# Optimization experiments

Hardware: AMD Instinct MI355X
Metric: run time of the kernel (lower is better)

Reference implementation:

```python
import jax, jax.numpy as jnp
import numpy as np

B, S, E, H = 2, 2048, 1024, 16
Dh = E // H  # 64
KEEP = 0.9   # 1 - dropout_p
INV_SCALE = 1.0  # forward() default; call site does not pass inv_scale


def setup_inputs() -> dict:
    key = jax.random.key(0)
    ks = jax.random.split(key, 12)
    query = jax.random.normal(ks[0], (B, S, E), dtype=jnp.float32)
    key_t = jax.random.normal(ks[1], (B, S, E), dtype=jnp.float32)
    value = jax.random.normal(ks[2], (B, S, E), dtype=jnp.float32)
    attn_mask = jax.random.randint(ks[3], (B, S), 0, 2, dtype=jnp.int32)
    # pre-scaled inverted dropout keep-mask (deterministic stand-in for F.dropout)
    dropout_mask = (jax.random.uniform(ks[4], (B, H, S, S)) < KEEP).astype(jnp.float32) / KEEP
    Wq = jax.random.normal(ks[5], (E, E), dtype=jnp.float32) * 0.02
    bq = jnp.zeros((E,), dtype=jnp.float32)
    Wk = jax.random.normal(ks[6], (E, E), dtype=jnp.float32) * 0.02
    bk = jnp.zeros((E,), dtype=jnp.float32)
    Wv = jax.random.normal(ks[7], (E, E), dtype=jnp.float32) * 0.02
    bv = jnp.zeros((E,), dtype=jnp.float32)
    return {"query": query, "key": key_t, "value": value, "attn_mask": attn_mask,
            "dropout_mask": dropout_mask, "Wq": Wq, "bq": bq, "Wk": Wk, "bk": bk,
            "Wv": Wv, "bv": bv}


def _heads(x, W, b):
    # Linear then split heads: (B,S,E) -> (B,H,S,Dh)
    y = x @ W.T + b
    return y.reshape(B, S, H, Dh).transpose(0, 2, 1, 3)


def reference(query, key, value, attn_mask, dropout_mask, Wq, bq, Wk, bk, Wv, bv):
    q = _heads(query, Wq, bq)
    k = _heads(key, Wk, bk)
    v = _heads(value, Wv, bv)
    scores = jnp.einsum("bhqd,bhkd->bhqk", q, k) / INV_SCALE
    pad = (attn_mask == 0)[:, None, None, :]  # (B,1,1,S) True = masked
    scores = jnp.where(pad, -jnp.inf, scores)
    attn = jax.nn.softmax(scores, axis=-1) * dropout_mask
    out = jnp.einsum("bhqk,bhkd->bhqd", attn, v)  # (B,H,S,Dh)
    return out
```

## Files before the change

### kernel.cpp

```cpp
#include <hip/hip_runtime.h>

#define B_ 2
#define S_ 2048
#define E_ 1024
#define H_ 16
#define DH 64
#define MM (B_*S_)
#define BHN (B_*H_)

typedef unsigned short u16;
typedef unsigned int u32;
typedef __attribute__((ext_vector_type(8))) __bf16 bf16x8;
typedef __attribute__((ext_vector_type(4))) float f32x4;
typedef __attribute__((ext_vector_type(8))) u16 u16x8;
typedef __attribute__((ext_vector_type(4))) u16 u16x4;

static __device__ __forceinline__ u16 f2bf(float f) {
  u32 u = __builtin_bit_cast(u32, f);
  u += 0x7fffu + ((u >> 16) & 1u);
  return (u16)(u >> 16);
}
static __device__ __forceinline__ float bf2f(u16 h) {
  return __builtin_bit_cast(float, (u32)h << 16);
}
static __device__ __forceinline__ u32 sw(u32 byte) {
  return byte ^ (((byte >> 7) & 7u) << 4);
}
static __device__ __forceinline__ void cp16(u16* lds, u32 ldsbyte, const u16* g) {
  *(u16x8*)((char*)lds + ldsbyte) = *(const u16x8*)g;
}
static __device__ __forceinline__ bf16x8 frag(const u16* lds, u32 byte) {
  return *(const bf16x8*)((const char*)lds + byte);
}
static __device__ __forceinline__ f32x4 mfma16(bf16x8 a, bf16x8 b, f32x4 c) {
  return __builtin_amdgcn_mfma_f32_16x16x32_bf16(a, b, c, 0, 0, 0);
}

__global__ void split3_kernel(const float* __restrict__ s0, u16* __restrict__ h0, u16* __restrict__ l0,
                              const float* __restrict__ s1, u16* __restrict__ h1, u16* __restrict__ l1,
                              const float* __restrict__ s2, u16* __restrict__ h2, u16* __restrict__ l2,
                              int n4) {
  const float* src = (blockIdx.z == 0) ? s0 : (blockIdx.z == 1) ? s1 : s2;
  u16* hi = (blockIdx.z == 0) ? h0 : (blockIdx.z == 1) ? h1 : h2;
  u16* lo = (blockIdx.z == 0) ? l0 : (blockIdx.z == 1) ? l1 : l2;
  int i = blockIdx.x * blockDim.x + threadIdx.x;
  int stride = gridDim.x * blockDim.x;
  for (; i < n4; i += stride) {
    float4 v = ((const float4*)src)[i];
    u16x4 h, l;
    h.x = f2bf(v.x); l.x = f2bf(v.x - bf2f(h.x));
    h.y = f2bf(v.y); l.y = f2bf(v.y - bf2f(h.y));
    h.z = f2bf(v.z); l.z = f2bf(v.z - bf2f(h.z));
    h.w = f2bf(v.w); l.w = f2bf(v.w - bf2f(h.w));
    ((u16x4*)hi)[i] = h;
    ((u16x4*)lo)[i] = l;
  }
}

struct ProjArgs {
  const u16* xhi; const u16* xlo; const u16* whi; const u16* wlo;
  const float* bias; u16* ohi; u16* olo; int mode;
};

__global__ __launch_bounds__(256, 2) void proj_gemm(ProjArgs a0, ProjArgs a1, ProjArgs a2) {
  ProjArgs A = (blockIdx.z == 0) ? a0 : (blockIdx.z == 1) ? a1 : a2;
  __shared__ u16 As[128 * 64];
  __shared__ u16 Bs[128 * 64];
  const int t = threadIdx.x;
  const int l = t & 63, wid = t >> 6;
  const int g = l >> 4, ln = l & 15;
  const int wm = wid >> 1, wn = wid & 1;
  const int m0 = blockIdx.y * 128, e0 = blockIdx.x * 128;

  f32x4 acc[4][4] = {};

  for (int kt = 0; kt < 48; ++kt) {
    int kp = kt * 64;
    const u16* asrc = (kp < 2048) ? A.xhi : A.xlo;
    const u16* bsrc = (kp < 1024 || kp >= 2048) ? A.whi : A.wlo;
    int kc = kp & 1023;
#pragma unroll
    for (int i = 0; i < 4; ++i) {
      int c = t + 256 * i;
      int row = c >> 3;
      u32 lb = sw((u32)c * 16);
      cp16(As, lb, asrc + (size_t)(m0 + row) * 1024 + kc + (c & 7) * 8);
      cp16(Bs, lb, bsrc + (size_t)(e0 + row) * 1024 + kc + (c & 7) * 8);
    }
    __syncthreads();
#pragma unroll
    for (int ks = 0; ks < 2; ++ks) {
      bf16x8 af[4], bfv[4];
#pragma unroll
      for (int i = 0; i < 4; ++i) {
        u32 ar = (u32)(wm * 64 + i * 16 + ln);
        af[i] = frag(As, sw(ar * 128 + g * 16 + ks * 64));
        u32 br = (u32)(wn * 64 + i * 16 + ln);
        bfv[i] = frag(Bs, sw(br * 128 + g * 16 + ks * 64));
      }
#pragma unroll
      for (int i = 0; i < 4; ++i)
#pragma unroll
        for (int j = 0; j < 4; ++j)
          acc[i][j] = mfma16(af[i], bfv[j], acc[i][j]);
    }
    __syncthreads();
  }

#pragma unroll
  for (int i = 0; i < 4; ++i) {
#pragma unroll
    for (int j = 0; j < 4; ++j) {
      int e = e0 + wn * 64 + j * 16 + ln;
      int h = e >> 6, d = e & 63;
      float bias = A.bias[e];
      if (A.mode < 2) {
#pragma unroll
        for (int r = 0; r < 4; ++r) {
          int m = m0 + wm * 64 + i * 16 + g * 4 + r;
          float v = acc[i][j][r] + bias;
          int b = m >> 11, s = m & 2047;
          size_t idx = ((size_t)((b * 16 + h) * 2048 + s)) * 64 + d;
          u16 hv = f2bf(v);
          A.ohi[idx] = hv;
          A.olo[idx] = f2bf(v - bf2f(hv));
        }
      } else {
        int m = m0 + wm * 64 + i * 16 + g * 4;
        int b = m >> 11, s = m & 2047;
        u16x4 pv;
#pragma unroll
        for (int r = 0; r < 4; ++r) pv[r] = f2bf(acc[i][j][r] + bias);
        size_t idx = ((size_t)((b * 16 + h) * 64 + d)) * 2048 + s;
        *(u16x4*)(A.ohi + idx) = pv;
      }
    }
  }
}

__global__ __launch_bounds__(256, 4) void attn_kernel(
    const u16* __restrict__ qhi, const u16* __restrict__ qlo,
    const u16* __restrict__ khi, const u16* __restrict__ klo,
    const u16* __restrict__ vt, const int* __restrict__ amask,
    const float* __restrict__ dmask, float* __restrict__ out) {
  __shared__ u16 Ksh[64 * 64];
  __shared__ u16 Ksl[64 * 64];
  __shared__ u16 Vs[64 * 64];
  __shared__ u16 Ps[4 * 16 * 64];

  const int t = threadIdx.x, l = t & 63, wid = t >> 6;
  const int g = l >> 4, ln = l & 15;

  int bid = blockIdx.y * 32 + blockIdx.x;
  int sid = (bid & 7) * 128 + (bid >> 3);
  const int qt = sid & 31, bh = sid >> 5, b = bh >> 4;
  const int q0 = qt * 64;
  const int qrow = q0 + wid * 16 + ln;
  const size_t qg = ((size_t)bh * 2048 + qrow) * 64;

  bf16x8 qh[2], ql[2];
#pragma unroll
  for (int ks = 0; ks < 2; ++ks) {
    qh[ks] = *(const bf16x8*)(qhi + qg + ks * 32 + g * 8);
    ql[ks] = *(const bf16x8*)(qlo + qg + ks * 32 + g * 8);
  }

  f32x4 O[4] = {};
  float Zacc = 0.f;
  const size_t dmrow = ((size_t)bh * 2048 + qrow) * 2048;
  const u32 psbase = (u32)(wid * 2048 + ln * 128);

  for (int kt = 0; kt < 32; ++kt) {
    const int k0 = kt * 64;
    float4 dm[4]; int4 ok[4];
#pragma unroll
    for (int i = 0; i < 4; ++i) {
      dm[i] = *(const float4*)(dmask + dmrow + k0 + i * 16 + 4 * g);
      ok[i] = *(const int4*)(amask + b * 2048 + k0 + i * 16 + 4 * g);
    }

    if (kt) __syncthreads();
    const size_t kbase = ((size_t)bh * 2048 + k0) * 64;
#pragma unroll
    for (int i = 0; i < 2; ++i) {
      int c = t + 256 * i;
      u32 lb = sw((u32)c * 16);
      int row = c >> 3;
      cp16(Ksh, lb, khi + kbase + c * 8);
      cp16(Ksl, lb, klo + kbase + c * 8);
      cp16(Vs, lb, vt + ((size_t)bh * 64 + row) * 2048 + k0 + (c & 7) * 8);
    }
    __syncthreads();

    f32x4 sc[4] = {};
#pragma unroll
    for (int ks = 0; ks < 2; ++ks) {
#pragma unroll
      for (int i = 0; i < 4; ++i) {
        u32 byt = sw((u32)((i * 16 + ln) * 128 + ks * 64 + g * 16));
        bf16x8 akh = frag(Ksh, byt);
        bf16x8 akl = frag(Ksl, byt);
        sc[i] = mfma16(akh, qh[ks], sc[i]);
        sc[i] = mfma16(akh, ql[ks], sc[i]);
        sc[i] = mfma16(akl, qh[ks], sc[i]);
      }
    }

#pragma unroll
    for (int i = 0; i < 4; ++i) {
      float e0 = ok[i].x ? __expf(sc[i][0]) : 0.f;
      float e1 = ok[i].y ? __expf(sc[i][1]) : 0.f;
      float e2 = ok[i].z ? __expf(sc[i][2]) : 0.f;
      float e3 = ok[i].w ? __expf(sc[i][3]) : 0.f;
      Zacc += (e0 + e1) + (e2 + e3);
      u16x4 p;
      p.x = f2bf(e0 * dm[i].x);
      p.y = f2bf(e1 * dm[i].y);
      p.z = f2bf(e2 * dm[i].z);
      p.w = f2bf(e3 * dm[i].w);
      *(u16x4*)((char*)Ps + sw(psbase + i * 32 + g * 8)) = p;
    }

#pragma unroll
    for (int ks = 0; ks < 2; ++ks) {
      bf16x8 bP = frag(Ps, sw(psbase + ks * 64 + g * 16));
#pragma unroll
      for (int id = 0; id < 4; ++id) {
        bf16x8 aV = frag(Vs, sw((u32)((id * 16 + ln) * 128 + ks * 64 + g * 16)));
        O[id] = mfma16(aV, bP, O[id]);
      }
    }
  }

  float z = Zacc;
  z += __shfl_xor(z, 16, 64);
  z += __shfl_xor(z, 32, 64);
  float rz = 1.f / z;

#pragma unroll
  for (int id = 0; id < 4; ++id) {
    float4 o;
    o.x = O[id][0] * rz; o.y = O[id][1] * rz;
    o.z = O[id][2] * rz; o.w = O[id][3] * rz;
    *(float4*)(out + qg + id * 16 + 4 * g) = o;
  }
}

extern "C" void kernel_launch(void* const* d_in, const int* in_sizes, int n_in,
                              void* d_out, int out_size, void* d_ws, size_t ws_size,
                              hipStream_t stream) {
  const float* query = (const float*)d_in[0];
  const float* keyt  = (const float*)d_in[1];
  const float* value = (const float*)d_in[2];
  const int*   amask = (const int*)d_in[3];
  const float* dmask = (const float*)d_in[4];
  const float* Wq = (const float*)d_in[5];
  const float* bq = (const float*)d_in[6];
  const float* Wk = (const float*)d_in[7];
  const float* bk = (const float*)d_in[8];
  const float* Wv = (const float*)d_in[9];
  const float* bv = (const float*)d_in[10];

  char* ws = (char*)d_ws;
  size_t off = 0;
  auto alloc = [&](size_t bytes) {
    char* p = ws + off;
    off += (bytes + 255) & ~(size_t)255;
    return p;
  };
  const size_t XB = (size_t)MM * E_ * sizeof(u16);
  const size_t WB = (size_t)E_ * E_ * sizeof(u16);

  u16 *xh[3], *xl[3], *wh[3], *wl[3];
  for (int i = 0; i < 3; ++i) { xh[i] = (u16*)alloc(XB); xl[i] = (u16*)alloc(XB); }
  for (int i = 0; i < 3; ++i) { wh[i] = (u16*)alloc(WB); wl[i] = (u16*)alloc(WB); }
  u16* q_hi = (u16*)alloc(XB);
  u16* q_lo = (u16*)alloc(XB);
  u16* k_hi = (u16*)alloc(XB);
  u16* k_lo = (u16*)alloc(XB);
  u16* v_t  = (u16*)alloc(XB);
  if (off > ws_size) return;

  split3_kernel<<<dim3(1024, 1, 3), 256, 0, stream>>>(
      query, xh[0], xl[0], keyt, xh[1], xl[1], value, xh[2], xl[2], MM * E_ / 4);
  split3_kernel<<<dim3(256, 1, 3), 256, 0, stream>>>(
      Wq, wh[0], wl[0], Wk, wh[1], wl[1], Wv, wh[2], wl[2], E_ * E_ / 4);

  ProjArgs pa[3] = {
      {xh[0], xl[0], wh[0], wl[0], bq, q_hi, q_lo, 0},
      {xh[1], xl[1], wh[1], wl[1], bk, k_hi, k_lo, 1},
      {xh[2], xl[2], wh[2], wl[2], bv, v_t, nullptr, 2},
  };
  proj_gemm<<<dim3(E_ / 128, MM / 128, 3), 256, 0, stream>>>(pa[0], pa[1], pa[2]);

  attn_kernel<<<dim3(32, 32), 256, 0, stream>>>(
      q_hi, q_lo, k_hi, k_lo, v_t, amask, dmask, (float*)d_out);
}
```

Baseline: 328.7 us.

## Prefetch attention tiles, use global_load_lds in projection, merge split launches

The attention kernel now double-buffers K/V tiles through registers, loading the next tile while computing the current one, and its occupancy hint drops from 4 to 3. The projection GEMM uses direct global-to-LDS loads without the swizzle, remaps block IDs for locality, and skips the low-precision pass for the V projection (32 k-tiles instead of 48). The two split kernels merge into one launch. The unswizzled LDS layout may cause bank conflicts, and dropping V's lo term lowers accuracy.

Measured after the change: 306.4 us. 1.07x faster.

```diff
diff --git a/kernel.cpp b/kernel.cpp
--- a/kernel.cpp
+++ b/kernel.cpp
@@ -26,34 +26,35 @@
 static __device__ __forceinline__ u32 sw(u32 byte) {
   return byte ^ (((byte >> 7) & 7u) << 4);
 }
-static __device__ __forceinline__ void cp16(u16* lds, u32 ldsbyte, const u16* g) {
-  *(u16x8*)((char*)lds + ldsbyte) = *(const u16x8*)g;
-}
 static __device__ __forceinline__ bf16x8 frag(const u16* lds, u32 byte) {
   return *(const bf16x8*)((const char*)lds + byte);
 }
 static __device__ __forceinline__ f32x4 mfma16(bf16x8 a, bf16x8 b, f32x4 c) {
   return __builtin_amdgcn_mfma_f32_16x16x32_bf16(a, b, c, 0, 0, 0);
 }
-
-__global__ void split3_kernel(const float* __restrict__ s0, u16* __restrict__ h0, u16* __restrict__ l0,
-                              const float* __restrict__ s1, u16* __restrict__ h1, u16* __restrict__ l1,
-                              const float* __restrict__ s2, u16* __restrict__ h2, u16* __restrict__ l2,
-                              int n4) {
-  const float* src = (blockIdx.z == 0) ? s0 : (blockIdx.z == 1) ? s1 : s2;
-  u16* hi = (blockIdx.z == 0) ? h0 : (blockIdx.z == 1) ? h1 : h2;
-  u16* lo = (blockIdx.z == 0) ? l0 : (blockIdx.z == 1) ? l1 : l2;
+static __device__ __forceinline__ void gload_lds16(const u16* g, u16* lds_base) {
+  __builtin_amdgcn_global_load_lds(
+      (const __attribute__((address_space(1))) u32*)g,
+      (__attribute__((address_space(3))) u32*)lds_base, 16, 0, 0);
+}
+
+struct SplitArg { const float* s; u16* h; u16* l; int n4; };
+
+__global__ void split6_kernel(SplitArg a0, SplitArg a1, SplitArg a2,
+                              SplitArg a3, SplitArg a4, SplitArg a5) {
+  SplitArg A = (blockIdx.z == 0) ? a0 : (blockIdx.z == 1) ? a1 : (blockIdx.z == 2) ? a2
+             : (blockIdx.z == 3) ? a3 : (blockIdx.z == 4) ? a4 : a5;
   int i = blockIdx.x * blockDim.x + threadIdx.x;
   int stride = gridDim.x * blockDim.x;
-  for (; i < n4; i += stride) {
-    float4 v = ((const float4*)src)[i];
+  for (; i < A.n4; i += stride) {
+    float4 v = ((const float4*)A.s)[i];
     u16x4 h, l;
     h.x = f2bf(v.x); l.x = f2bf(v.x - bf2f(h.x));
     h.y = f2bf(v.y); l.y = f2bf(v.y - bf2f(h.y));
     h.z = f2bf(v.z); l.z = f2bf(v.z - bf2f(h.z));
     h.w = f2bf(v.w); l.w = f2bf(v.w - bf2f(h.w));
-    ((u16x4*)hi)[i] = h;
-    ((u16x4*)lo)[i] = l;
+    ((u16x4*)A.h)[i] = h;
+    ((u16x4*)A.l)[i] = l;
   }
 }
 
@@ -70,22 +71,25 @@
   const int l = t & 63, wid = t >> 6;
   const int g = l >> 4, ln = l & 15;
   const int wm = wid >> 1, wn = wid & 1;
-  const int m0 = blockIdx.y * 128, e0 = blockIdx.x * 128;
+  int bid = blockIdx.y * 8 + blockIdx.x;
+  int sid = (bid & 7) * 32 + (bid >> 3);
+  const int m0 = (sid >> 3) * 128, e0 = (sid & 7) * 128;
 
   f32x4 acc[4][4] = {};
-
-  for (int kt = 0; kt < 48; ++kt) {
+  const int nkt = (A.mode == 2) ? 32 : 48;
+
+  for (int kt = 0; kt < nkt; ++kt) {
     int kp = kt * 64;
     const u16* asrc = (kp < 2048) ? A.xhi : A.xlo;
     const u16* bsrc = (kp < 1024 || kp >= 2048) ? A.whi : A.wlo;
     int kc = kp & 1023;
 #pragma unroll
-    for (int i = 0; i < 4; ++i) {
-      int c = t + 256 * i;
-      int row = c >> 3;
-      u32 lb = sw((u32)c * 16);
-      cp16(As, lb, asrc + (size_t)(m0 + row) * 1024 + kc + (c & 7) * 8);
-      cp16(Bs, lb, bsrc + (size_t)(e0 + row) * 1024 + kc + (c & 7) * 8);
+    for (int r = 0; r < 4; ++r) {
+      int cr = wid * 4 + r;
+      int row = cr * 8 + (l >> 3);
+      int col = (l & 7) * 8;
+      gload_lds16(asrc + (size_t)(m0 + row) * 1024 + kc + col, As + cr * 512);
+      gload_lds16(bsrc + (size_t)(e0 + row) * 1024 + kc + col, Bs + cr * 512);
     }
     __syncthreads();
 #pragma unroll
@@ -93,10 +97,8 @@
       bf16x8 af[4], bfv[4];
 #pragma unroll
       for (int i = 0; i < 4; ++i) {
-        u32 ar = (u32)(wm * 64 + i * 16 + ln);
-        af[i] = frag(As, sw(ar * 128 + g * 16 + ks * 64));
-        u32 br = (u32)(wn * 64 + i * 16 + ln);
-        bfv[i] = frag(Bs, sw(br * 128 + g * 16 + ks * 64));
+        af[i] = frag(As, (u32)(wm * 64 + i * 16 + ln) * 128 + ks * 64 + g * 16);
+        bfv[i] = frag(Bs, (u32)(wn * 64 + i * 16 + ln) * 128 + ks * 64 + g * 16);
       }
 #pragma unroll
       for (int i = 0; i < 4; ++i)
@@ -138,7 +140,7 @@
   }
 }
 
-__global__ __launch_bounds__(256, 4) void attn_kernel(
+__global__ __launch_bounds__(256, 3) void attn_kernel(
     const u16* __restrict__ qhi, const u16* __restrict__ qlo,
     const u16* __restrict__ khi, const u16* __restrict__ klo,
     const u16* __restrict__ vt, const int* __restrict__ amask,
@@ -165,6 +167,34 @@
     ql[ks] = *(const bf16x8*)(qlo + qg + ks * 32 + g * 8);
   }
 
+  u16x8 rkh[2], rkl[2], rv[2];
+  auto load_tile = [&](int kt) {
+    const int k0 = kt * 64;
+    const size_t kbase = ((size_t)bh * 2048 + k0) * 64;
+#pragma unroll
+    for (int i = 0; i < 2; ++i) {
+      int c = t + 256 * i;
+      rkh[i] = *(const u16x8*)(khi + kbase + c * 8);
+      rkl[i] = *(const u16x8*)(klo + kbase + c * 8);
+      int row = c >> 3;
+      rv[i] = *(const u16x8*)(vt + ((size_t)bh * 64 + row) * 2048 + k0 + (c & 7) * 8);
+    }
+  };
+  auto write_tile = [&]() {
+#pragma unroll
+    for (int i = 0; i < 2; ++i) {
+      int c = t + 256 * i;
+      u32 lb = sw((u32)c * 16);
+      *(u16x8*)((char*)Ksh + lb) = rkh[i];
+      *(u16x8*)((char*)Ksl + lb) = rkl[i];
+      *(u16x8*)((char*)Vs + lb) = rv[i];
+    }
+  };
+
+  load_tile(0);
+  write_tile();
+  __syncthreads();
+
   f32x4 O[4] = {};
   float Zacc = 0.f;
   const size_t dmrow = ((size_t)bh * 2048 + qrow) * 2048;
@@ -172,25 +202,13 @@
 
   for (int kt = 0; kt < 32; ++kt) {
     const int k0 = kt * 64;
+    load_tile(kt < 31 ? kt + 1 : 31);
     float4 dm[4]; int4 ok[4];
 #pragma unroll
     for (int i = 0; i < 4; ++i) {
       dm[i] = *(const float4*)(dmask + dmrow + k0 + i * 16 + 4 * g);
       ok[i] = *(const int4*)(amask + b * 2048 + k0 + i * 16 + 4 * g);
     }
-
-    if (kt) __syncthreads();
-    const size_t kbase = ((size_t)bh * 2048 + k0) * 64;
-#pragma unroll
-    for (int i = 0; i < 2; ++i) {
-      int c = t + 256 * i;
-      u32 lb = sw((u32)c * 16);
-      int row = c >> 3;
-      cp16(Ksh, lb, khi + kbase + c * 8);
-      cp16(Ksl, lb, klo + kbase + c * 8);
-      cp16(Vs, lb, vt + ((size_t)bh * 64 + row) * 2048 + k0 + (c & 7) * 8);
-    }
-    __syncthreads();
 
     f32x4 sc[4] = {};
 #pragma unroll
@@ -229,6 +247,12 @@
         bf16x8 aV = frag(Vs, sw((u32)((id * 16 + ln) * 128 + ks * 64 + g * 16)));
         O[id] = mfma16(aV, bP, O[id]);
       }
+    }
+
+    __syncthreads();
+    if (kt < 31) {
+      write_tile();
+      __syncthreads();
     }
   }
 
@@ -281,17 +305,19 @@
   u16* v_t  = (u16*)alloc(XB);
   if (off > ws_size) return;
 
-  split3_kernel<<<dim3(1024, 1, 3), 256, 0, stream>>>(
-      query, xh[0], xl[0], keyt, xh[1], xl[1], value, xh[2], xl[2], MM * E_ / 4);
-  split3_kernel<<<dim3(256, 1, 3), 256, 0, stream>>>(
-      Wq, wh[0], wl[0], Wk, wh[1], wl[1], Wv, wh[2], wl[2], E_ * E_ / 4);
+  SplitArg sa[6] = {
+      {query, xh[0], xl[0], MM * E_ / 4}, {keyt, xh[1], xl[1], MM * E_ / 4},
+      {value, xh[2], xl[2], MM * E_ / 4}, {Wq, wh[0], wl[0], E_ * E_ / 4},
+      {Wk, wh[1], wl[1], E_ * E_ / 4},    {Wv, wh[2], wl[2], E_ * E_ / 4},
+  };
+  split6_kernel<<<dim3(512, 1, 6), 256, 0, stream>>>(sa[0], sa[1], sa[2], sa[3], sa[4], sa[5]);
 
   ProjArgs pa[3] = {
       {xh[0], xl[0], wh[0], wl[0], bq, q_hi, q_lo, 0},
       {xh[1], xl[1], wh[1], wl[1], bk, k_hi, k_lo, 1},
       {xh[2], xl[2], wh[2], wl[2], bv, v_t, nullptr, 2},
   };
-  proj_gemm<<<dim3(E_ / 128, MM / 128, 3), 256, 0, stream>>>(pa[0], pa[1], pa[2]);
+  proj_gemm<<<dim3(8, 32, 3), 256, 0, stream>>>(pa[0], pa[1], pa[2]);
 
   attn_kernel<<<dim3(32, 32), 256, 0, stream>>>(
       q_hi, q_lo, k_hi, k_lo, v_t, amask, dmask, (float*)d_out);
```
